# Optimization experiments

Measured on AMD Instinct MI355X. Metric: run time of the kernel, lower is better.

## Reference

```python
import jax
import jax.numpy as jnp
from jax import lax
import numpy as np

DIM = 256
WIN = 7


def setup_inputs() -> dict:
    key = jax.random.key(0)
    ks = jax.random.split(key, 7)
    B, C, H, W = 16, DIM, 64, 64
    k = WIN
    return {
        "x": jax.random.normal(ks[0], (B, C, H, W), dtype=jnp.float32),
        "dw_weight": jax.random.normal(ks[1], (C, 1, k, k), dtype=jnp.float32) * 0.1,
        "pw_weight": jax.random.normal(ks[2], (C, C), dtype=jnp.float32) * 0.05,
        "w1": jax.random.normal(ks[3], (C // 4, C), dtype=jnp.float32) * 0.05,
        "b1": jax.random.normal(ks[4], (C // 4,), dtype=jnp.float32) * 0.05,
        "w2": jax.random.normal(ks[5], (C * k * k, C // 4), dtype=jnp.float32) * 0.05,
        "b2": jax.random.normal(ks[6], (C * k * k,), dtype=jnp.float32) * 0.05,
    }


def reference(x, dw_weight, pw_weight, w1, b1, w2, b2):
    B, C, H, W = x.shape
    k = dw_weight.shape[-1]
    pad = k // 2
    # dynamic kernel generator: global avg pool -> 1x1 conv -> GELU -> 1x1 conv
    pooled = x.mean(axis=(2, 3))                                  # [B, C]
    h = jax.nn.gelu(pooled @ w1.T + b1, approximate=False)        # [B, C//4]
    dyn = (h @ w2.T + b2).reshape(B, C, 1, k, k)                  # [B, C, 1, k, k]
    # fuse static depthwise weights with dynamic per-sample weights
    fused = dw_weight[None] + dyn                                  # [B, C, 1, k, k]
    # per-instance depthwise conv via groups = B*C
    x_flat = x.reshape(1, B * C, H, W)
    kern = fused.reshape(B * C, 1, k, k)
    out = lax.conv_general_dilated(
        x_flat, kern,
        window_strides=(1, 1),
        padding=[(pad, pad), (pad, pad)],
        feature_group_count=B * C,
        dimension_numbers=("NCHW", "OIHW", "NCHW"),
    )
    out = out.reshape(B, C, H, W)
    # final 1x1 pointwise conv (no bias)
    return jnp.einsum("bchw,oc->bohw", out, pw_weight)
```

## Files before the change

### kernel.cpp

```cpp
#include <hip/hip_runtime.h>
#include <math.h>
#include <stdint.h>

typedef __attribute__((ext_vector_type(8))) short short8;
typedef __attribute__((ext_vector_type(4))) float f32x4;

#define B_  16
#define C_  256
#define HW_ 4096
#define KK_ 49
#define CR_ 64

__device__ __forceinline__ ushort f2bf(float f) {
    union { float f; uint32_t u; } v; v.f = f;
    uint32_t r = (v.u + 0x7FFFu + ((v.u >> 16) & 1u)) >> 16;
    return (ushort)r;
}

__global__ __launch_bounds__(256) void pool_kernel(const float* __restrict__ x,
                                                   float* __restrict__ pooled) {
    int bc = blockIdx.x;
    const float4* p4 = (const float4*)(x + (size_t)bc * HW_);
    float s = 0.f;
    for (int i = threadIdx.x; i < HW_ / 4; i += 256) {
        float4 v = p4[i];
        s += (v.x + v.y) + (v.z + v.w);
    }
#pragma unroll
    for (int off = 32; off > 0; off >>= 1) s += __shfl_down(s, off);
    __shared__ float red[4];
    if ((threadIdx.x & 63) == 0) red[threadIdx.x >> 6] = s;
    __syncthreads();
    if (threadIdx.x == 0)
        pooled[bc] = (red[0] + red[1] + red[2] + red[3]) * (1.f / HW_);
}

__global__ __launch_bounds__(64) void mlp_kernel(const float* __restrict__ pooled,
                                                 const float* __restrict__ w1,
                                                 const float* __restrict__ b1,
                                                 float* __restrict__ h) {
    int b = blockIdx.x;
    int r = threadIdx.x;
    __shared__ float pr[C_];
    for (int i = r; i < C_; i += 64) pr[i] = pooled[b * C_ + i];
    __syncthreads();
    float acc = b1[r];
    const float* wr = w1 + (size_t)r * C_;
    for (int c = 0; c < C_; c += 4) {
        float4 wv = *(const float4*)(wr + c);
        acc += pr[c] * wv.x + pr[c + 1] * wv.y + pr[c + 2] * wv.z + pr[c + 3] * wv.w;
    }
    h[b * CR_ + r] = 0.5f * acc * (1.f + erff(acc * 0.70710678118654752f));
}

__global__ __launch_bounds__(256) void genw_kernel(const float* __restrict__ h,
                                                   const float* __restrict__ w2,
                                                   const float* __restrict__ b2,
                                                   const float* __restrict__ dw,
                                                   float* __restrict__ fused) {
    __shared__ float hs[B_ * CR_];
    int m = blockIdx.x * 256 + threadIdx.x;
    for (int i = threadIdx.x; i < B_ * CR_; i += 256) hs[i] = h[i];
    float wrow[CR_];
    const float4* w4 = (const float4*)(w2 + (size_t)m * CR_);
#pragma unroll
    for (int i = 0; i < CR_ / 4; i++) {
        float4 v = w4[i];
        wrow[4 * i] = v.x; wrow[4 * i + 1] = v.y;
        wrow[4 * i + 2] = v.z; wrow[4 * i + 3] = v.w;
    }
    float base = b2[m] + dw[m];
    __syncthreads();
    for (int b = 0; b < B_; b++) {
        float acc = base;
        const float* hb = hs + b * CR_;
#pragma unroll
        for (int r = 0; r < CR_; r++) acc += hb[r] * wrow[r];
        fused[(size_t)b * (C_ * KK_) + m] = acc;
    }
}

__global__ __launch_bounds__(256) void prep_kernel(const float* __restrict__ pw,
                                                   ushort* __restrict__ Pa) {
    int idx = blockIdx.x * 256 + threadIdx.x;
    int o = idx >> 8, c = idx & 255;
    Pa[(size_t)(((o >> 4) * 32) + (c >> 3)) * 128 + (o & 15) * 8 + (c & 7)] = f2bf(pw[idx]);
}

__global__ __launch_bounds__(512, 4) void dw_kernel(const float* __restrict__ x,
                                                    const float* __restrict__ fused,
                                                    ushort* __restrict__ Ug) {
    __shared__ __align__(16) float xs[8 * 22 * 72];
    ushort* Us = (ushort*)xs;

    const int strip = blockIdx.x;
    const int cb    = blockIdx.y;
    const int b     = blockIdx.z;
    const int tid   = threadIdx.x;
    const int wid   = tid >> 6;
    const int lane  = tid & 63;
    const int c0    = cb * 8;
    const int r0    = strip * 16;

    {
        const float* xp = x + (((size_t)(b * C_ + c0 + wid)) << 12);
        float* xd = xs + wid * 1584;
#pragma unroll
        for (int row = 0; row < 22; row++) {
            int gr = r0 + row - 3;
            float v = 0.f;
            if ((unsigned)gr < 64u) v = xp[(gr << 6) + lane];
            xd[row * 72 + 3 + lane] = v;
        }
        for (int j = lane; j < 176; j += 64) {
            int row = j >> 3, e = j & 7;
            int col = (e < 3) ? e : (64 + e);
            xd[row * 72 + col] = 0.f;
        }
    }

    float wk[49];
    {
        const float* fp = fused + (((size_t)b * C_) + c0 + wid) * KK_;
        float v = (lane < KK_) ? fp[lane] : 0.f;
        int vi = __float_as_int(v);
#pragma unroll
        for (int t = 0; t < 49; t++) {
            wk[t] = __int_as_float(__builtin_amdgcn_readlane(vi, t));
            asm volatile("" : "+s"(wk[t]));
        }
    }
    __syncthreads();

    const int cg = lane & 15;
    const int rg = lane >> 4;
    float acc[4][4];
#pragma unroll
    for (int ro = 0; ro < 4; ro++)
#pragma unroll
        for (int co = 0; co < 4; co++) acc[ro][co] = 0.f;

    const float* xbase = xs + wid * 1584 + (rg * 4) * 72 + cg * 4;
#pragma unroll
    for (int rr = 0; rr < 10; rr++) {
        float xr[10];
        *(float4*)&xr[0] = *(const float4*)(xbase + rr * 72);
        *(float4*)&xr[4] = *(const float4*)(xbase + rr * 72 + 4);
        *(float2*)&xr[8] = *(const float2*)(xbase + rr * 72 + 8);
        const int olo = (rr - 6 < 0) ? 0 : rr - 6;
        const int ohi = (rr < 3) ? rr : 3;
#pragma unroll
        for (int ro = olo; ro <= ohi; ro++) {
            const int ki = rr - ro;
#pragma unroll
            for (int j = 0; j < 7; j++) {
#pragma unroll
                for (int co = 0; co < 4; co++)
                    acc[ro][co] = fmaf(xr[co + j], wk[ki * 7 + j], acc[ro][co]);
            }
        }
    }
    __syncthreads();

#pragma unroll
    for (int ro = 0; ro < 4; ro++) {
#pragma unroll
        for (int co = 0; co < 4; co++) {
            int o = rg * 4 + ro;
            int c = cg * 4 + co;
            int q = o * 4 + (c >> 4);
            int part = (c & 15) ^ (q & 15);
            Us[q * 128 + part * 8 + wid] = f2bf(acc[ro][co]);
        }
    }
    __syncthreads();

    for (int t = tid; t < 1024; t += 512) {
        int q = t >> 4, part = t & 15;
        int o = q >> 2, cgrp = q & 3;
        size_t e = ((((size_t)b * 256) + (size_t)((r0 + o) * 4 + cgrp)) * 32 + cb) * 128
                   + (size_t)part * 8;
        *(uint4*)(Ug + e) = *(const uint4*)(Us + q * 128 + ((part ^ (q & 15)) * 8));
    }
}

#define GLDS16(gp, lp) __builtin_amdgcn_global_load_lds(\
    (const __attribute__((address_space(1))) uint32_t*)(gp), \
    (__attribute__((address_space(3))) uint32_t*)(lp), 16, 0, 0)

__global__ __launch_bounds__(256, 2) void pw_kernel(const ushort* __restrict__ Pa,
                                                    const ushort* __restrict__ Ug,
                                                    float* __restrict__ Y) {
    __shared__ ushort As[2][8192];
    __shared__ ushort Bs[2][4096];
    const int pb   = blockIdx.x;
    const int b    = blockIdx.y;
    const int tid  = threadIdx.x;
    const int w    = tid >> 6;
    const int lane = tid & 63;
    const int oi   = lane & 15;
    const int kq   = lane >> 4;

    f32x4 acc[4][8];
#pragma unroll
    for (int mi = 0; mi < 4; mi++)
#pragma unroll
        for (int ni = 0; ni < 8; ni++)
            acc[mi][ni] = (f32x4){0.f, 0.f, 0.f, 0.f};

    const size_t ubase = (((size_t)b * 256) + (size_t)pb * 8) * 32 * 128;

#define STAGE(BUF, KB0)                                                          \
    for (int q = w; q < 24; q += 4) {                                            \
        const ushort* src; ushort* dst;                                          \
        if (q < 16) { src = Pa + ((size_t)q * 32 + (KB0)) * 128;                 \
                      dst = &As[BUF][q * 512]; }                                 \
        else { int pg = q - 16;                                                  \
               src = Ug + ubase + ((size_t)pg * 32 + (KB0)) * 128;               \
               dst = &Bs[BUF][pg * 512]; }                                       \
        GLDS16(src + lane * 8, dst);                                             \
    }

    STAGE(0, 0)

#pragma unroll
    for (int ki = 0; ki < 8; ki++) {
        const int buf = ki & 1;
        if (ki < 7) {
            STAGE(buf ^ 1, (ki + 1) * 4)
            asm volatile("s_waitcnt vmcnt(6)" ::: "memory");
        } else {
            asm volatile("s_waitcnt vmcnt(0)" ::: "memory");
        }
        __builtin_amdgcn_s_barrier();
        __builtin_amdgcn_sched_barrier(0);

        short8 af[4], bf[8];
#pragma unroll
        for (int mi = 0; mi < 4; mi++)
            af[mi] = *(const short8*)&As[buf][(w * 4 + mi) * 512 + kq * 128 + oi * 8];
#pragma unroll
        for (int ni = 0; ni < 8; ni++)
            bf[ni] = *(const short8*)&Bs[buf][ni * 512 + kq * 128 + oi * 8];
#pragma unroll
        for (int mi = 0; mi < 4; mi++)
#pragma unroll
            for (int ni = 0; ni < 8; ni++)
                acc[mi][ni] = __builtin_amdgcn_mfma_f32_16x16x32_bf16(
                    af[mi], bf[ni], acc[mi][ni], 0, 0, 0);

        __builtin_amdgcn_s_barrier();
        __builtin_amdgcn_sched_barrier(0);
    }

    float* yb = Y + ((size_t)b << 20);
    const int p0 = pb * 128;
#pragma unroll
    for (int mi = 0; mi < 4; mi++) {
#pragma unroll
        for (int ni = 0; ni < 8; ni++) {
            int p = p0 + ni * 16 + oi;
#pragma unroll
            for (int r = 0; r < 4; r++) {
                int o = w * 64 + mi * 16 + kq * 4 + r;
                yb[(size_t)o * HW_ + p] = acc[mi][ni][r];
            }
        }
    }
#undef STAGE
}

extern "C" void kernel_launch(void* const* d_in, const int* in_sizes, int n_in,
                              void* d_out, int out_size, void* d_ws, size_t ws_size,
                              hipStream_t stream) {
    const float* x  = (const float*)d_in[0];
    const float* dw = (const float*)d_in[1];
    const float* pw = (const float*)d_in[2];
    const float* w1 = (const float*)d_in[3];
    const float* b1 = (const float*)d_in[4];
    const float* w2 = (const float*)d_in[5];
    const float* b2 = (const float*)d_in[6];
    float* out = (float*)d_out;

    char* ws = (char*)d_ws;
    float*  pooled = (float*)(ws);
    float*  h      = (float*)(ws + 16384);
    float*  fused  = (float*)(ws + 20480);
    ushort* Pa     = (ushort*)(ws + 823296);
    ushort* Ug     = (ushort*)(ws + 1048576);

    hipLaunchKernelGGL(pool_kernel, dim3(B_ * C_), dim3(256), 0, stream, x, pooled);
    hipLaunchKernelGGL(mlp_kernel,  dim3(B_), dim3(64), 0, stream, pooled, w1, b1, h);
    hipLaunchKernelGGL(genw_kernel, dim3(49), dim3(256), 0, stream, h, w2, b2, dw, fused);
    hipLaunchKernelGGL(prep_kernel, dim3(256), dim3(256), 0, stream, pw, Pa);
    hipLaunchKernelGGL(dw_kernel,   dim3(4, 32, B_), dim3(512), 0, stream, x, fused, Ug);
    hipLaunchKernelGGL(pw_kernel,   dim3(32, B_), dim3(256), 0, stream, Pa, Ug, out);
}
```

Baseline: 102.8 us.

## Fuse MLP into weight generator, halve depthwise channel block, load tile via LDS DMA

Merges the small MLP kernel into the dynamic-weight generator so each of the 49 blocks recomputes the GELU hidden layer from the pooled vector, removing one launch at the cost of redundant MLP work per block. The depthwise kernel now processes 4 channels per 256-thread block instead of 8 per 512, doubling the grid and cutting LDS per block. The input tile is staged with global_load_lds direct-to-LDS copies, and the output staging drops the XOR swizzle for half-width uint2 stores into the interleaved bf16 layout.

```diff
diff --git a/kernel.cpp b/kernel.cpp
--- a/kernel.cpp
+++ b/kernel.cpp
@@ -16,6 +16,13 @@
     uint32_t r = (v.u + 0x7FFFu + ((v.u >> 16) & 1u)) >> 16;
     return (ushort)r;
 }
+
+#define GLDS16(gp, lp) __builtin_amdgcn_global_load_lds(\
+    (const __attribute__((address_space(1))) uint32_t*)(gp), \
+    (__attribute__((address_space(3))) uint32_t*)(lp), 16, 0, 0)
+#define GLDS4(gp, lp) __builtin_amdgcn_global_load_lds(\
+    (const __attribute__((address_space(1))) uint32_t*)(gp), \
+    (__attribute__((address_space(3))) uint32_t*)(lp), 4, 0, 0)
 
 __global__ __launch_bounds__(256) void pool_kernel(const float* __restrict__ x,
                                                    float* __restrict__ pooled) {
@@ -35,32 +42,32 @@
         pooled[bc] = (red[0] + red[1] + red[2] + red[3]) * (1.f / HW_);
 }
 
-__global__ __launch_bounds__(64) void mlp_kernel(const float* __restrict__ pooled,
-                                                 const float* __restrict__ w1,
-                                                 const float* __restrict__ b1,
-                                                 float* __restrict__ h) {
-    int b = blockIdx.x;
-    int r = threadIdx.x;
-    __shared__ float pr[C_];
-    for (int i = r; i < C_; i += 64) pr[i] = pooled[b * C_ + i];
-    __syncthreads();
-    float acc = b1[r];
-    const float* wr = w1 + (size_t)r * C_;
-    for (int c = 0; c < C_; c += 4) {
-        float4 wv = *(const float4*)(wr + c);
-        acc += pr[c] * wv.x + pr[c + 1] * wv.y + pr[c + 2] * wv.z + pr[c + 3] * wv.w;
-    }
-    h[b * CR_ + r] = 0.5f * acc * (1.f + erff(acc * 0.70710678118654752f));
-}
-
-__global__ __launch_bounds__(256) void genw_kernel(const float* __restrict__ h,
-                                                   const float* __restrict__ w2,
-                                                   const float* __restrict__ b2,
-                                                   const float* __restrict__ dw,
-                                                   float* __restrict__ fused) {
+__global__ __launch_bounds__(256) void mlpgenw_kernel(const float* __restrict__ pooled,
+                                                      const float* __restrict__ w1,
+                                                      const float* __restrict__ b1,
+                                                      const float* __restrict__ w2,
+                                                      const float* __restrict__ b2,
+                                                      const float* __restrict__ dwt,
+                                                      float* __restrict__ fused) {
+    __shared__ float ps[B_ * C_];
     __shared__ float hs[B_ * CR_];
-    int m = blockIdx.x * 256 + threadIdx.x;
-    for (int i = threadIdx.x; i < B_ * CR_; i += 256) hs[i] = h[i];
+    const int tid = threadIdx.x;
+    for (int i = tid; i < B_ * C_; i += 256) ps[i] = pooled[i];
+    __syncthreads();
+    for (int v = tid; v < B_ * CR_; v += 256) {
+        int b = v >> 6, r = v & 63;
+        float acc = b1[r];
+        const float* wr = w1 + (size_t)r * C_;
+        const float* pb = ps + b * C_;
+        for (int c = 0; c < C_; c += 4) {
+            float4 wv = *(const float4*)(wr + c);
+            acc += pb[c] * wv.x + pb[c + 1] * wv.y + pb[c + 2] * wv.z + pb[c + 3] * wv.w;
+        }
+        hs[v] = 0.5f * acc * (1.f + erff(acc * 0.70710678118654752f));
+    }
+    __syncthreads();
+
+    int m = blockIdx.x * 256 + tid;
     float wrow[CR_];
     const float4* w4 = (const float4*)(w2 + (size_t)m * CR_);
 #pragma unroll
@@ -69,8 +76,7 @@
         wrow[4 * i] = v.x; wrow[4 * i + 1] = v.y;
         wrow[4 * i + 2] = v.z; wrow[4 * i + 3] = v.w;
     }
-    float base = b2[m] + dw[m];
-    __syncthreads();
+    float base = b2[m] + dwt[m];
     for (int b = 0; b < B_; b++) {
         float acc = base;
         const float* hb = hs + b * CR_;
@@ -87,10 +93,10 @@
     Pa[(size_t)(((o >> 4) * 32) + (c >> 3)) * 128 + (o & 15) * 8 + (c & 7)] = f2bf(pw[idx]);
 }
 
-__global__ __launch_bounds__(512, 4) void dw_kernel(const float* __restrict__ x,
+__global__ __launch_bounds__(256, 4) void dw_kernel(const float* __restrict__ x,
                                                     const float* __restrict__ fused,
                                                     ushort* __restrict__ Ug) {
-    __shared__ __align__(16) float xs[8 * 22 * 72];
+    __shared__ __align__(16) float xs[4 * 22 * 72];
     ushort* Us = (ushort*)xs;
 
     const int strip = blockIdx.x;
@@ -99,7 +105,7 @@
     const int tid   = threadIdx.x;
     const int wid   = tid >> 6;
     const int lane  = tid & 63;
-    const int c0    = cb * 8;
+    const int c0    = cb * 4;
     const int r0    = strip * 16;
 
     {
@@ -108,9 +114,12 @@
 #pragma unroll
         for (int row = 0; row < 22; row++) {
             int gr = r0 + row - 3;
-            float v = 0.f;
-            if ((unsigned)gr < 64u) v = xp[(gr << 6) + lane];
-            xd[row * 72 + 3 + lane] = v;
+            if ((unsigned)gr < 64u) {
+                GLDS4(xp + (gr << 6) + lane, xd + row * 72 + 3);
+            } else if (lane < 36) {
+                xd[row * 72 + 2 * lane] = 0.f;
+                xd[row * 72 + 2 * lane + 1] = 0.f;
+            }
         }
         for (int j = lane; j < 176; j += 64) {
             int row = j >> 3, e = j & 7;
@@ -168,25 +177,19 @@
         for (int co = 0; co < 4; co++) {
             int o = rg * 4 + ro;
             int c = cg * 4 + co;
-            int q = o * 4 + (c >> 4);
-            int part = (c & 15) ^ (q & 15);
-            Us[q * 128 + part * 8 + wid] = f2bf(acc[ro][co]);
-        }
-    }
-    __syncthreads();
-
-    for (int t = tid; t < 1024; t += 512) {
+            Us[(o * 4 + (c >> 4)) * 64 + (c & 15) * 4 + wid] = f2bf(acc[ro][co]);
+        }
+    }
+    __syncthreads();
+
+    for (int t = tid; t < 1024; t += 256) {
         int q = t >> 4, part = t & 15;
         int o = q >> 2, cgrp = q & 3;
-        size_t e = ((((size_t)b * 256) + (size_t)((r0 + o) * 4 + cgrp)) * 32 + cb) * 128
-                   + (size_t)part * 8;
-        *(uint4*)(Ug + e) = *(const uint4*)(Us + q * 128 + ((part ^ (q & 15)) * 8));
-    }
-}
-
-#define GLDS16(gp, lp) __builtin_amdgcn_global_load_lds(\
-    (const __attribute__((address_space(1))) uint32_t*)(gp), \
-    (__attribute__((address_space(3))) uint32_t*)(lp), 16, 0, 0)
+        size_t e = ((((size_t)b * 256) + (size_t)((r0 + o) * 4 + cgrp)) * 32 + (cb >> 1)) * 128
+                   + (size_t)part * 8 + (cb & 1) * 4;
+        *(uint2*)(Ug + e) = *(const uint2*)(Us + q * 64 + part * 4);
+    }
+}
 
 __global__ __launch_bounds__(256, 2) void pw_kernel(const ushort* __restrict__ Pa,
                                                     const ushort* __restrict__ Ug,
@@ -284,15 +287,14 @@
 
     char* ws = (char*)d_ws;
     float*  pooled = (float*)(ws);
-    float*  h      = (float*)(ws + 16384);
-    float*  fused  = (float*)(ws + 20480);
-    ushort* Pa     = (ushort*)(ws + 823296);
+    float*  fused  = (float*)(ws + 16384);
+    ushort* Pa     = (ushort*)(ws + 819200);
     ushort* Ug     = (ushort*)(ws + 1048576);
 
-    hipLaunchKernelGGL(pool_kernel, dim3(B_ * C_), dim3(256), 0, stream, x, pooled);
-    hipLaunchKernelGGL(mlp_kernel,  dim3(B_), dim3(64), 0, stream, pooled, w1, b1, h);
-    hipLaunchKernelGGL(genw_kernel, dim3(49), dim3(256), 0, stream, h, w2, b2, dw, fused);
-    hipLaunchKernelGGL(prep_kernel, dim3(256), dim3(256), 0, stream, pw, Pa);
-    hipLaunchKernelGGL(dw_kernel,   dim3(4, 32, B_), dim3(512), 0, stream, x, fused, Ug);
-    hipLaunchKernelGGL(pw_kernel,   dim3(32, B_), dim3(256), 0, stream, Pa, Ug, out);
-}
+    hipLaunchKernelGGL(pool_kernel,    dim3(B_ * C_), dim3(256), 0, stream, x, pooled);
+    hipLaunchKernelGGL(mlpgenw_kernel, dim3(49), dim3(256), 0, stream,
+                       pooled, w1, b1, w2, b2, dw, fused);
+    hipLaunchKernelGGL(prep_kernel,    dim3(256), dim3(256), 0, stream, pw, Pa);
+    hipLaunchKernelGGL(dw_kernel,      dim3(4, 64, B_), dim3(256), 0, stream, x, fused, Ug);
+    hipLaunchKernelGGL(pw_kernel,      dim3(32, B_), dim3(256), 0, stream, Pa, Ug, out);
+}
```

After: 105.3 us. 2.5% more time.
